# Kernel optimization log

Measured on AMD Instinct MI355X. Metric: run time of the kernel, lower is better.

## Reference

```python
import math
import jax, jax.numpy as jnp
import numpy as np

MAX_ATOMS_PER_BB = 8

def _sinusoidal_pe(d_model, max_len):
    # Faithful port of SinusoidalPositionalEmbedding buffer construction.
    position = jnp.arange(max_len, dtype=jnp.float32)[:, None]          # (L,1)
    div_term = jnp.exp(jnp.arange(0, d_model, 2, dtype=jnp.float32) * -(math.log(10000.0) / d_model))
    n_even = math.ceil(d_model / 2)
    n_odd = d_model - n_even
    pe = jnp.zeros((max_len, d_model), dtype=jnp.float32)
    pe = pe.at[:, 0::2].set(jnp.sin(position * div_term[:n_even]))
    pe = pe.at[:, 1::2].set(jnp.cos(position * div_term[:n_odd]))
    return pe

def setup_inputs() -> dict:
    key = jax.random.key(0)
    k1, k2, k3, k4 = jax.random.split(key, 4)
    bs, n, dy, dc = 8, 32, 64, 256
    E = jax.random.normal(k1, (bs, n, n, dy), dtype=jnp.float32)
    e_mask1 = (jax.random.uniform(k2, (bs, n, 1, 1)) > 0.2).astype(jnp.float32)
    e_mask2 = (jax.random.uniform(k3, (bs, 1, n, 1)) > 0.2).astype(jnp.float32)
    W = jax.random.normal(k4, (dc, dy), dtype=jnp.float32) * (1.0 / math.sqrt(dy))
    return {"E": E, "e_mask1": e_mask1, "e_mask2": e_mask2, "W": W}

def reference(E, e_mask1, e_mask2, W):
    M = MAX_ATOMS_PER_BB
    bs, n, _, dy = E.shape
    nm = n * M
    # Positional embedding table indexed by arange(M*M).reshape(M,M) -> (M,M,dy)
    pe = _sinusoidal_pe(dy, M * M).reshape(M, M, dy)
    # Masks: note original flattening orders (n,M) for mask1 but (M,n) for mask2.
    mask1 = jnp.broadcast_to(e_mask1, (bs, n, M, 1)).reshape(bs, nm, 1, 1)
    mask2 = jnp.broadcast_to(e_mask2, (bs, M, n, 1)).reshape(bs, 1, nm, 1)
    mask = mask1 * mask2                                             # (bs,nm,nm,1)
    # Broadcast E (bs,n,1,n,1,dy) + pe (1,1,M,1,M,dy) -> (bs,n,M,n,M,dy)
    Eb = E[:, :, None, :, None, :] + pe[None, None, :, None, :, :]
    E_masked = Eb.reshape(bs, nm, nm, dy) * mask
    out = jnp.einsum('bijd,cd->bijc', E_masked, W)                    # (bs,nm,nm,dc)
    return out
```

## Files before the change

kernel.cpp:

```cpp
#include <hip/hip_runtime.h>
#include <math.h>


__global__ __launch_bounds__(256) void cpe_kernel(const float* __restrict__ W,
                                                  float* __restrict__ Cpe) {
    const int pos = blockIdx.x;
    const int t   = threadIdx.x;
    __shared__ float peL[64];
    if (t < 64) {
        const float k2  = (float)(t & ~1);
        const float div = expf(-k2 * (logf(10000.0f) / 64.0f));
        const float arg = (float)pos * div;
        peL[t] = (t & 1) ? cosf(arg) : sinf(arg);
    }
    __syncthreads();
    const float4* W4 = (const float4*)W;
    float acc = 0.0f;
#pragma unroll
    for (int d4 = 0; d4 < 16; ++d4) {
        float4 w = W4[t * 16 + d4];
        acc += w.x * peL[4 * d4 + 0] + w.y * peL[4 * d4 + 1] +
               w.z * peL[4 * d4 + 2] + w.w * peL[4 * d4 + 3];
    }
    Cpe[pos * 256 + t] = acc;
}

__global__ __launch_bounds__(256) void etoc_kernel(const float* __restrict__ E,
                                                   const float* __restrict__ m1p,
                                                   const float* __restrict__ m2p,
                                                   const float* __restrict__ W,
                                                   const float* __restrict__ Cpe,
                                                   float* __restrict__ out) {
    const int blk = blockIdx.x;
    const int j = blk & 31;
    const int i = (blk >> 5) & 31;
    const int b = blk >> 10;
    const int t = threadIdx.x;

    __shared__ float Ev[64];
    __shared__ float ceS[256];
    __shared__ float m2s[8];

    if (t < 64) {
        Ev[t] = E[((size_t)((b * 32 + i) * 32 + j) << 6) + t];
    }
    if (t >= 64 && t < 72) {
        m2s[t - 64] = m2p[b * 32 + ((j & 3) << 3) + (t - 64)];
    }
    __syncthreads();

    {
        const float4* W4 = (const float4*)W;
        float acc = 0.0f;
#pragma unroll
        for (int d4 = 0; d4 < 16; ++d4) {
            float4 w = W4[t * 16 + d4];
            acc += w.x * Ev[4 * d4 + 0] + w.y * Ev[4 * d4 + 1] +
                   w.z * Ev[4 * d4 + 2] + w.w * Ev[4 * d4 + 3];
        }
        ceS[t] = acc;
    }
    __syncthreads();

    const float m1 = m1p[b * 32 + i];
    const int w = t >> 6;
    const int g = t & 63;

    const float4 ce4 = ((const float4*)ceS)[g];
    const float4* Cpe4 = (const float4*)Cpe;
    float4* out4 = (float4*)out;

    const size_t rowBase = (((size_t)b * 256 + (size_t)i * 8) * 256 + (size_t)j * 8);

#pragma unroll
    for (int p0 = 0; p0 < 16; ++p0) {
        const int p = w * 16 + p0;
        const int a = p >> 3;
        const int c = p & 7;
        const float m = m1 * m2s[c];
        const float4 q = Cpe4[p * 64 + g];
        float4 r;
        r.x = (ce4.x + q.x) * m;
        r.y = (ce4.y + q.y) * m;
        r.z = (ce4.z + q.z) * m;
        r.w = (ce4.w + q.w) * m;
        const size_t idx = (rowBase + (size_t)a * 256 + (size_t)c) * 64 + (size_t)g;
        out4[idx] = r;
    }
}

extern "C" void kernel_launch(void* const* d_in, const int* in_sizes, int n_in,
                              void* d_out, int out_size, void* d_ws, size_t ws_size,
                              hipStream_t stream) {
    const float* E   = (const float*)d_in[0];
    const float* m1p = (const float*)d_in[1];
    const float* m2p = (const float*)d_in[2];
    const float* W   = (const float*)d_in[3];
    float* out = (float*)d_out;
    float* Cpe = (float*)d_ws;

    cpe_kernel<<<64, 256, 0, stream>>>(W, Cpe);
    etoc_kernel<<<8192, 256, 0, stream>>>(E, m1p, m2p, W, Cpe, out);
}
```

Measured before the change: 126.9 us.

## Coarsen output blocks over four columns and use nontemporal stores

Each block now handles four adjacent j positions instead of one. W is loaded into registers once and reused for four E·W dot products, and each Cpe load is shared across four outputs. Output writes use nontemporal stores to avoid polluting caches for the large streaming write. This gives 4x fewer blocks with more registers per thread, which may reduce occupancy.

```diff
diff --git a/kernel.cpp b/kernel.cpp
--- a/kernel.cpp
+++ b/kernel.cpp
@@ -1,5 +1,7 @@
 #include <hip/hip_runtime.h>
 #include <math.h>
+
+typedef float f32x4 __attribute__((ext_vector_type(4)));
 
 
 __global__ __launch_bounds__(256) void cpe_kernel(const float* __restrict__ W,
@@ -14,11 +16,11 @@
         peL[t] = (t & 1) ? cosf(arg) : sinf(arg);
     }
     __syncthreads();
-    const float4* W4 = (const float4*)W;
+    const f32x4* W4 = (const f32x4*)W;
     float acc = 0.0f;
 #pragma unroll
     for (int d4 = 0; d4 < 16; ++d4) {
-        float4 w = W4[t * 16 + d4];
+        f32x4 w = W4[t * 16 + d4];
         acc += w.x * peL[4 * d4 + 0] + w.y * peL[4 * d4 + 1] +
                w.z * peL[4 * d4 + 2] + w.w * peL[4 * d4 + 3];
     }
@@ -32,60 +34,64 @@
                                                    const float* __restrict__ Cpe,
                                                    float* __restrict__ out) {
     const int blk = blockIdx.x;
-    const int j = blk & 31;
-    const int i = (blk >> 5) & 31;
-    const int b = blk >> 10;
-    const int t = threadIdx.x;
+    const int jg = blk & 7;
+    const int i  = (blk >> 3) & 31;
+    const int b  = blk >> 8;
+    const int t  = threadIdx.x;
 
-    __shared__ float Ev[64];
-    __shared__ float ceS[256];
-    __shared__ float m2s[8];
+    __shared__ float Ev[4 * 64];
+    __shared__ float ceS[4 * 256];
+    __shared__ float m2s[32];
 
-    if (t < 64) {
-        Ev[t] = E[((size_t)((b * 32 + i) * 32 + j) << 6) + t];
-    }
-    if (t >= 64 && t < 72) {
-        m2s[t - 64] = m2p[b * 32 + ((j & 3) << 3) + (t - 64)];
+    Ev[t] = E[((size_t)((b * 32 + i) * 32 + jg * 4) << 6) + t];
+    if (t < 32) m2s[t] = m2p[b * 32 + t];
+    __syncthreads();
+
+    {
+        const f32x4* W4 = (const f32x4*)W;
+        f32x4 wr[16];
+#pragma unroll
+        for (int d4 = 0; d4 < 16; ++d4) wr[d4] = W4[t * 16 + d4];
+#pragma unroll
+        for (int dj = 0; dj < 4; ++dj) {
+            const float* e = &Ev[dj * 64];
+            float acc = 0.0f;
+#pragma unroll
+            for (int d4 = 0; d4 < 16; ++d4) {
+                acc += wr[d4].x * e[4 * d4 + 0] + wr[d4].y * e[4 * d4 + 1] +
+                       wr[d4].z * e[4 * d4 + 2] + wr[d4].w * e[4 * d4 + 3];
+            }
+            ceS[dj * 256 + t] = acc;
+        }
     }
     __syncthreads();
 
-    {
-        const float4* W4 = (const float4*)W;
-        float acc = 0.0f;
-#pragma unroll
-        for (int d4 = 0; d4 < 16; ++d4) {
-            float4 w = W4[t * 16 + d4];
-            acc += w.x * Ev[4 * d4 + 0] + w.y * Ev[4 * d4 + 1] +
-                   w.z * Ev[4 * d4 + 2] + w.w * Ev[4 * d4 + 3];
-        }
-        ceS[t] = acc;
-    }
-    __syncthreads();
-
-    const float m1 = m1p[b * 32 + i];
+    const float m1v = m1p[b * 32 + i];
     const int w = t >> 6;
     const int g = t & 63;
 
-    const float4 ce4 = ((const float4*)ceS)[g];
-    const float4* Cpe4 = (const float4*)Cpe;
-    float4* out4 = (float4*)out;
+    f32x4 ce4[4];
+#pragma unroll
+    for (int dj = 0; dj < 4; ++dj) ce4[dj] = ((const f32x4*)(ceS + dj * 256))[g];
 
-    const size_t rowBase = (((size_t)b * 256 + (size_t)i * 8) * 256 + (size_t)j * 8);
+    const f32x4* Cpe4 = (const f32x4*)Cpe;
+    f32x4* out4 = (f32x4*)out;
+
+    const size_t base = (((size_t)(b * 256 + i * 8) * 256) + (size_t)jg * 32) * 64 + (size_t)g;
 
 #pragma unroll
     for (int p0 = 0; p0 < 16; ++p0) {
         const int p = w * 16 + p0;
         const int a = p >> 3;
         const int c = p & 7;
-        const float m = m1 * m2s[c];
-        const float4 q = Cpe4[p * 64 + g];
-        float4 r;
-        r.x = (ce4.x + q.x) * m;
-        r.y = (ce4.y + q.y) * m;
-        r.z = (ce4.z + q.z) * m;
-        r.w = (ce4.w + q.w) * m;
-        const size_t idx = (rowBase + (size_t)a * 256 + (size_t)c) * 64 + (size_t)g;
-        out4[idx] = r;
+        const f32x4 q = Cpe4[p * 64 + g];
+        const size_t idxA = base + (size_t)a * 16384 + (size_t)c * 64;
+#pragma unroll
+        for (int dj = 0; dj < 4; ++dj) {
+            const float m = m1v * m2s[dj * 8 + c];
+            f32x4 r = (ce4[dj] + q) * m;
+            __builtin_nontemporal_store(r, &out4[idxA + (size_t)dj * 512]);
+        }
     }
 }
 
@@ -100,5 +106,5 @@
     float* Cpe = (float*)d_ws;
 
     cpe_kernel<<<64, 256, 0, stream>>>(W, Cpe);
-    etoc_kernel<<<8192, 256, 0, stream>>>(E, m1p, m2p, W, Cpe, out);
+    etoc_kernel<<<2048, 256, 0, stream>>>(E, m1p, m2p, W, Cpe, out);
 }
```

Result: faster. 114.3 us (-9.9%).
